# Kernel tuning notes

Measured on AMD Instinct MI355X. Metric: run time of the kernel, lower is better.

Reference implementation:

```python
import jax, jax.numpy as jnp
import numpy as np

N, E, DIN, H, EIN, EH, STEPS = 10000, 100000, 64, 64, 16, 128, 3


def setup_inputs() -> dict:
    key = jax.random.key(0)
    ks = jax.random.split(key, 8)
    n_feat = jax.random.normal(ks[0], (N, DIN), jnp.float32)
    e_feat = jax.random.normal(ks[1], (E, EIN), jnp.float32)
    src = jax.random.randint(ks[2], (E,), 0, N, jnp.int32)
    dst = jax.random.randint(ks[3], (E,), 0, N, jnp.int32)
    W0 = jax.random.normal(ks[4], (DIN, H), jnp.float32) / np.sqrt(DIN)
    b0 = jnp.zeros((H,), jnp.float32)
    We1 = jax.random.normal(ks[5], (EIN, EH), jnp.float32) / np.sqrt(EIN)
    be1 = jnp.zeros((EH,), jnp.float32)
    # small scale so per-edge HxH weight matrices keep activations stable
    We2 = jax.random.normal(ks[6], (EH, H * H), jnp.float32) * 0.02
    be2 = jnp.zeros((H * H,), jnp.float32)
    conv_bias = jnp.zeros((H,), jnp.float32)
    gamma = jnp.ones((H,), jnp.float32)
    beta = jnp.zeros((H,), jnp.float32)
    return {"n_feat": n_feat, "e_feat": e_feat, "src": src, "dst": dst,
            "W0": W0, "b0": b0, "We1": We1, "be1": be1, "We2": We2,
            "be2": be2, "conv_bias": conv_bias, "gamma": gamma, "beta": beta}


def reference(n_feat, e_feat, src, dst, W0, b0, We1, be1, We2, be2, conv_bias, gamma, beta):
    n = n_feat.shape[0]
    h = W0.shape[1]
    out = jax.nn.relu(n_feat @ W0 + b0)  # [N,H]
    # edge network (eval mode: dropout = identity); e_feat is fixed so the
    # per-edge weight matrices are identical each step -> compute once.
    w_edge = (jax.nn.relu(e_feat @ We1 + be1) @ We2 + be2).reshape(-1, h, h)  # [E,H,H]
    for _ in range(STEPS):
        msg = jnp.einsum('ei,eio->eo', out[src], w_edge)  # gather + per-edge matmul
        agg = jax.ops.segment_sum(msg, dst, num_segments=n)  # scatter-sum to dst
        out = jax.nn.relu(agg + conv_bias)
    # BatchNorm1d over nodes (training-mode batch statistics)
    mean = jnp.mean(out, axis=0)
    var = jnp.var(out, axis=0)
    return (out - mean) * jax.lax.rsqrt(var + 1e-5) * gamma + beta
```

## Files before the change

kernel.cpp:

```cpp
#include <hip/hip_runtime.h>
#include <stdint.h>

#define DIN   64
#define HDIM  64
#define EIN   16
#define EHID  128
#define HH    4096
#define TC    8256
#define STEPS 3

typedef short bf16x8 __attribute__((ext_vector_type(8)));
typedef float f32x4  __attribute__((ext_vector_type(4)));

__device__ __forceinline__ unsigned short f32_to_bf16(float f) {
    union { float f; uint32_t u; } v; v.f = f;
    uint32_t r = v.u + 0x7fffu + ((v.u >> 16) & 1u);
    return (unsigned short)(r >> 16);
}
__device__ __forceinline__ float bfu_to_f(unsigned short u) {
    union { uint32_t u; float f; } v; v.u = (uint32_t)u << 16; return v.f;
}

__global__ void k_node_mlp(const float* __restrict__ nf, const float* __restrict__ W0,
                           const float* __restrict__ b0, float* __restrict__ outb,
                           unsigned short* __restrict__ outbf, int n_nodes) {
    __shared__ float w0s[DIN * HDIM];
    int tid = threadIdx.x;
    for (int i = tid; i < DIN * HDIM; i += 256) w0s[i] = W0[i];
    __syncthreads();
    int node = blockIdx.x * 4 + (tid >> 6);
    int o = tid & 63;
    if (node >= n_nodes) return;
    float xr = nf[node * DIN + o];
    float acc = b0[o];
#pragma unroll 8
    for (int i = 0; i < DIN; ++i)
        acc += __shfl(xr, i, 64) * w0s[i * HDIM + o];
    float v = fmaxf(acc, 0.f);
    outb[node * HDIM + o] = v;
    outbf[node * HDIM + o] = f32_to_bf16(v);
}

__global__ void k_edge_mlp(const float* __restrict__ ef, const float* __restrict__ We1,
                           const float* __restrict__ be1, unsigned short* __restrict__ h, int n_edges) {
    __shared__ float w1s[EIN * EHID];
    __shared__ float xs[16 * EIN];
    int t = threadIdx.x;
    int e0 = blockIdx.x * 16;
#pragma unroll
    for (int i = t; i < EIN * EHID; i += 256) w1s[i] = We1[i];
    xs[t] = ef[(size_t)e0 * EIN + t];
    __syncthreads();
    int g = t >> 4, c0 = (t & 15) * 8;
    int edge = e0 + g;
    if (edge >= n_edges) return;
    float acc[8];
#pragma unroll
    for (int j = 0; j < 8; ++j) acc[j] = be1[c0 + j];
#pragma unroll
    for (int i = 0; i < EIN; ++i) {
        float xi = xs[g * EIN + i];
#pragma unroll
        for (int j = 0; j < 8; ++j) acc[j] += xi * w1s[i * EHID + c0 + j];
    }
    uint32_t p0 = f32_to_bf16(fmaxf(acc[0], 0.f)) | ((uint32_t)f32_to_bf16(fmaxf(acc[1], 0.f)) << 16);
    uint32_t p1 = f32_to_bf16(fmaxf(acc[2], 0.f)) | ((uint32_t)f32_to_bf16(fmaxf(acc[3], 0.f)) << 16);
    uint32_t p2 = f32_to_bf16(fmaxf(acc[4], 0.f)) | ((uint32_t)f32_to_bf16(fmaxf(acc[5], 0.f)) << 16);
    uint32_t p3 = f32_to_bf16(fmaxf(acc[6], 0.f)) | ((uint32_t)f32_to_bf16(fmaxf(acc[7], 0.f)) << 16);
    uint4 pk = {p0, p1, p2, p3};
    *(uint4*)(h + (size_t)edge * EHID + c0) = pk;
}

__global__ void k_bmat(const float* __restrict__ We2, const float* __restrict__ be2,
                       unsigned short* __restrict__ BmatT) {
    int t = blockIdx.x * 256 + threadIdx.x;
    if (t >= TC * 64) return;
    int c = t >> 6, i = t & 63;
    int g = c & 63;
    int m = (c & ~63) + 4 * (g & 15) + (g >> 4);
    float v;
    if (m < 8192) {
        int k = ((m >> 11) << 5) | (m & 31);
        int o = (m >> 5) & 63;
        v = We2[k * HH + i * 64 + o];
    } else {
        v = be2[i * 64 + (m - 8192)];
    }
    BmatT[t] = f32_to_bf16(v);
}

__global__ void k_T(const unsigned short* __restrict__ outbf, const unsigned short* __restrict__ BmatT,
                    unsigned short* __restrict__ T, int n0, int n1) {
    int wave = threadIdx.x >> 6, lane = threadIdx.x & 63;
    int r = lane & 15, q = lane >> 4;
    int eb = n0 + blockIdx.y * 64;
    int cb = blockIdx.x * 256 + wave * 64;
    f32x4 acc[4][4] = {};
#pragma unroll
    for (int s = 0; s < 2; ++s) {
        bf16x8 afr[4], bfr[4];
#pragma unroll
        for (int mt = 0; mt < 4; ++mt) {
            int e = eb + mt * 16 + r;
            if (e >= n1) e = n1 - 1;
            afr[mt] = *(const bf16x8*)(outbf + (size_t)e * 64 + s * 32 + q * 8);
        }
#pragma unroll
        for (int nt = 0; nt < 4; ++nt) {
            int c = cb + nt * 16 + r;
            if (c >= TC) c = 0;
            bfr[nt] = *(const bf16x8*)(BmatT + (size_t)c * 64 + s * 32 + q * 8);
        }
#pragma unroll
        for (int mt = 0; mt < 4; ++mt)
#pragma unroll
            for (int nt = 0; nt < 4; ++nt)
                acc[mt][nt] = __builtin_amdgcn_mfma_f32_16x16x32_bf16(afr[mt], bfr[nt], acc[mt][nt], 0, 0, 0);
    }
    if (cb >= TC) return;
#pragma unroll
    for (int mt = 0; mt < 4; ++mt)
#pragma unroll
        for (int rg = 0; rg < 4; ++rg) {
            int n = eb + mt * 16 + q * 4 + rg;
            if (n >= n1) continue;
            ushort4 pk;
            pk.x = f32_to_bf16(acc[mt][0][rg]);
            pk.y = f32_to_bf16(acc[mt][1][rg]);
            pk.z = f32_to_bf16(acc[mt][2][rg]);
            pk.w = f32_to_bf16(acc[mt][3][rg]);
            *(ushort4*)(T + (size_t)(n - n0) * TC + cb + 4 * r) = pk;
        }
}

__global__ void k_msg(const unsigned short* __restrict__ h, const unsigned short* __restrict__ T,
                      const int* __restrict__ offS, const int* __restrict__ permS,
                      float* __restrict__ msg, int n0, int n1) {
    int wave = threadIdx.x >> 6, lane = threadIdx.x & 63;
    int n = n0 + blockIdx.x * 4 + wave;
    if (n >= n1) return;
    int beg = offS[n], end = offS[n + 1];
    if (beg == end) return;
    int r = lane & 15, q = lane >> 4;
    const unsigned short* Tb = T + (size_t)(n - n0) * TC;
    float bias[4];
#pragma unroll
    for (int nt = 0; nt < 4; ++nt)
        bias[nt] = bfu_to_f(Tb[8192 + nt * 16 + r]);
    for (int j0 = beg; j0 < end; j0 += 16) {
        int jc = j0 + r; if (jc >= end) jc = end - 1;
        int e = permS[jc];
        const unsigned short* he = h + (size_t)e * EHID;
        f32x4 acc[4] = {};
#pragma unroll
        for (int s = 0; s < 4; ++s) {
            bf16x8 afr = *(const bf16x8*)(he + s * 32 + q * 8);
#pragma unroll
            for (int nt = 0; nt < 4; ++nt) {
                bf16x8 bfr = *(const bf16x8*)(Tb + s * 2048 + (nt * 16 + r) * 32 + q * 8);
                acc[nt] = __builtin_amdgcn_mfma_f32_16x16x32_bf16(afr, bfr, acc[nt], 0, 0, 0);
            }
        }
#pragma unroll
        for (int rg = 0; rg < 4; ++rg) {
            int jr = j0 + q * 4 + rg;
            if (jr >= end) continue;
            int er = permS[jr];
#pragma unroll
            for (int nt = 0; nt < 4; ++nt)
                msg[(size_t)er * 64 + nt * 16 + r] = acc[nt][rg] + bias[nt];
        }
    }
}

__global__ void k_hist(const int* __restrict__ src, const int* __restrict__ dst,
                       int* __restrict__ cntS, int* __restrict__ cntD, int n_edges) {
    int e = blockIdx.x * 256 + threadIdx.x;
    if (e >= n_edges) return;
    atomicAdd(&cntS[src[e]], 1);
    atomicAdd(&cntD[dst[e]], 1);
}

__global__ void k_scan(const int* __restrict__ cntS, const int* __restrict__ cntD,
                       int* __restrict__ offS, int* __restrict__ offD,
                       int* __restrict__ curS, int* __restrict__ curD, int n, int total) {
    const int* cnt = blockIdx.x ? cntD : cntS;
    int* off = blockIdx.x ? offD : offS;
    int* cur = blockIdx.x ? curD : curS;
    __shared__ int part[256];
    int tid = threadIdx.x;
    int chunk = (n + 255) / 256;
    int c0 = tid * chunk, c1 = c0 + chunk; if (c1 > n) c1 = n; if (c0 > n) c0 = n;
    int s = 0;
    for (int i = c0; i < c1; ++i) s += cnt[i];
    part[tid] = s;
    __syncthreads();
    for (int st = 1; st < 256; st <<= 1) {
        int v = (tid >= st) ? part[tid - st] : 0;
        __syncthreads();
        part[tid] += v;
        __syncthreads();
    }
    int run = tid ? part[tid - 1] : 0;
    for (int i = c0; i < c1; ++i) { off[i] = run; cur[i] = run; run += cnt[i]; }
    if (tid == 0) off[n] = total;
}

__global__ void k_perm(const int* __restrict__ src, const int* __restrict__ dst,
                       int* __restrict__ curS, int* __restrict__ curD,
                       int* __restrict__ permS, int* __restrict__ permD, int n_edges) {
    int e = blockIdx.x * 256 + threadIdx.x;
    if (e >= n_edges) return;
    permS[atomicAdd(&curS[src[e]], 1)] = e;
    permD[atomicAdd(&curD[dst[e]], 1)] = e;
}

__global__ void k_agg(const float* __restrict__ msg, const int* __restrict__ offD,
                      const int* __restrict__ permD, const float* __restrict__ cbias,
                      float* __restrict__ outb, unsigned short* __restrict__ outbf, int n_nodes) {
    int wave = threadIdx.x >> 6, lane = threadIdx.x & 63;
    int d = blockIdx.x * 4 + wave;
    if (d >= n_nodes) return;
    float acc = 0.f;
    int end = offD[d + 1];
    for (int j = offD[d]; j < end; ++j)
        acc += msg[(size_t)permD[j] * 64 + lane];
    float v = fmaxf(acc + cbias[lane], 0.f);
    outb[(size_t)d * 64 + lane] = v;
    outbf[(size_t)d * 64 + lane] = f32_to_bf16(v);
}

__global__ void k_bn_stats(const float* __restrict__ out, float* __restrict__ stat, int n_nodes) {
    __shared__ float s1[256], s2[256];
    int tid = threadIdx.x;
    int f = tid & 63, g = tid >> 6;
    float sum = 0.f, ss = 0.f;
    for (int r = blockIdx.x * 4 + g; r < n_nodes; r += 256) {
        float v = out[r * HDIM + f];
        sum += v; ss += v * v;
    }
    s1[tid] = sum; s2[tid] = ss;
    __syncthreads();
    if (tid < 64) {
        float A = s1[tid] + s1[64 + tid] + s1[128 + tid] + s1[192 + tid];
        float B = s2[tid] + s2[64 + tid] + s2[128 + tid] + s2[192 + tid];
        atomicAdd(&stat[tid], A);
        atomicAdd(&stat[64 + tid], B);
    }
}

__global__ void k_bn_final(const float* __restrict__ stat, const float* __restrict__ gamma,
                           const float* __restrict__ beta, float* __restrict__ sc, int n_nodes) {
    int f = threadIdx.x;
    if (f >= 64) return;
    float mean = stat[f] / n_nodes;
    float var  = stat[64 + f] / n_nodes - mean * mean;
    float inv  = rsqrtf(var + 1e-5f);
    float scale = gamma[f] * inv;
    sc[f] = scale;
    sc[64 + f] = beta[f] - mean * scale;
}

__global__ void k_bn_apply(const float* __restrict__ out, const float* __restrict__ sc,
                           float* __restrict__ y, int n) {
    int t = blockIdx.x * 256 + threadIdx.x;
    if (t >= n) return;
    int f = t & 63;
    y[t] = out[t] * sc[f] + sc[64 + f];
}

extern "C" void kernel_launch(void* const* d_in, const int* in_sizes, int n_in,
                              void* d_out, int out_size, void* d_ws, size_t ws_size,
                              hipStream_t stream) {
    const float* nf    = (const float*)d_in[0];
    const float* ef    = (const float*)d_in[1];
    const int*   src   = (const int*)d_in[2];
    const int*   dst   = (const int*)d_in[3];
    const float* W0    = (const float*)d_in[4];
    const float* b0    = (const float*)d_in[5];
    const float* We1   = (const float*)d_in[6];
    const float* be1   = (const float*)d_in[7];
    const float* We2   = (const float*)d_in[8];
    const float* be2   = (const float*)d_in[9];
    const float* cbias = (const float*)d_in[10];
    const float* gamma = (const float*)d_in[11];
    const float* beta  = (const float*)d_in[12];
    (void)n_in; (void)out_size;

    int n_nodes = in_sizes[0] / DIN;
    int n_edges = in_sizes[2];

    char* ws = (char*)d_ws;
    size_t off = 0;
    auto carve = [&](size_t bytes) -> void* {
        void* p = ws + off;
        off = (off + bytes + 255) & ~(size_t)255;
        return p;
    };
    unsigned short* h     = (unsigned short*)carve((size_t)n_edges * EHID * 2);
    float*          msg   = (float*)carve((size_t)n_edges * 64 * 4);
    float*          outb  = (float*)carve((size_t)n_nodes * HDIM * 4);
    unsigned short* outbf = (unsigned short*)carve((size_t)n_nodes * HDIM * 2);
    unsigned short* BmatT = (unsigned short*)carve((size_t)TC * 64 * 2);
    int*            offS  = (int*)carve((size_t)(n_nodes + 1) * 4);
    int*            offD  = (int*)carve((size_t)(n_nodes + 1) * 4);
    int*            curS  = (int*)carve((size_t)n_nodes * 4);
    int*            curD  = (int*)carve((size_t)n_nodes * 4);
    int*            permS = (int*)carve((size_t)n_edges * 4);
    int*            permD = (int*)carve((size_t)n_edges * 4);
    float*          stat  = (float*)carve(128 * 4 + (size_t)2 * n_nodes * 4);
    int*            cntS  = (int*)(stat + 128);
    int*            cntD  = cntS + n_nodes;
    float*          sc    = (float*)carve(128 * 4);
    unsigned short* T     = (unsigned short*)(ws + off);
    size_t avail = ws_size > off ? ws_size - off : 0;
    long tcap = (long)(avail / ((size_t)TC * 2));
    if (tcap > n_nodes) tcap = n_nodes;
    if (tcap < 64) tcap = 64;
    long half = (((long)n_nodes + 1) / 2 + 63) & ~63L;
    long tchunk = tcap < half ? tcap : half;

    hipMemsetAsync(stat, 0, 128 * 4 + (size_t)2 * n_nodes * 4, stream);

    k_node_mlp<<<dim3((n_nodes + 3) / 4), 256, 0, stream>>>(nf, W0, b0, outb, outbf, n_nodes);
    k_edge_mlp<<<dim3((n_edges + 15) / 16), 256, 0, stream>>>(ef, We1, be1, h, n_edges);
    k_bmat<<<dim3((TC * 64 + 255) / 256), 256, 0, stream>>>(We2, be2, BmatT);
    k_hist<<<dim3((n_edges + 255) / 256), 256, 0, stream>>>(src, dst, cntS, cntD, n_edges);
    k_scan<<<dim3(2), 256, 0, stream>>>(cntS, cntD, offS, offD, curS, curD, n_nodes, n_edges);
    k_perm<<<dim3((n_edges + 255) / 256), 256, 0, stream>>>(src, dst, curS, curD, permS, permD, n_edges);

    for (int step = 0; step < STEPS; ++step) {
        for (long n0 = 0; n0 < n_nodes; n0 += tchunk) {
            long n1 = n0 + tchunk; if (n1 > n_nodes) n1 = n_nodes;
            long cnt = n1 - n0;
            k_T<<<dim3((TC + 255) / 256, (cnt + 63) / 64), 256, 0, stream>>>(
                outbf, BmatT, T, (int)n0, (int)n1);
            k_msg<<<dim3((cnt + 3) / 4), 256, 0, stream>>>(
                h, T, offS, permS, msg, (int)n0, (int)n1);
        }
        k_agg<<<dim3((n_nodes + 3) / 4), 256, 0, stream>>>(msg, offD, permD, cbias, outb, outbf, n_nodes);
    }

    k_bn_stats<<<dim3(64), 256, 0, stream>>>(outb, stat, n_nodes);
    k_bn_final<<<dim3(1), 64, 0, stream>>>(stat, gamma, beta, sc, n_nodes);
    k_bn_apply<<<dim3((n_nodes * HDIM + 255) / 256), 256, 0, stream>>>(
        outb, sc, (float*)d_out, n_nodes * HDIM);
}
```

Before: 512.4 us.

## Merge prologue kernels, fold BN finalize into apply, retile k_T

Folds the node MLP, edge MLP, weight-matrix repack and degree histogram into one launch that dispatches on block index, and folds the BatchNorm finalize kernel into the apply kernel. Together these drop four launches. k_T now keeps the B fragments in registers and loops over 128 rows per block (8 M-tiles) instead of 64. This halves the grid in y and reuses B loads across more rows, but the bigger blocks may leave some compute units idle.

```diff
diff --git a/kernel.cpp b/kernel.cpp
--- a/kernel.cpp
+++ b/kernel.cpp
@@ -21,116 +21,122 @@
     union { uint32_t u; float f; } v; v.u = (uint32_t)u << 16; return v.f;
 }
 
-__global__ void k_node_mlp(const float* __restrict__ nf, const float* __restrict__ W0,
-                           const float* __restrict__ b0, float* __restrict__ outb,
-                           unsigned short* __restrict__ outbf, int n_nodes) {
-    __shared__ float w0s[DIN * HDIM];
-    int tid = threadIdx.x;
-    for (int i = tid; i < DIN * HDIM; i += 256) w0s[i] = W0[i];
-    __syncthreads();
-    int node = blockIdx.x * 4 + (tid >> 6);
-    int o = tid & 63;
-    if (node >= n_nodes) return;
-    float xr = nf[node * DIN + o];
-    float acc = b0[o];
+__global__ void k_pro(const float* __restrict__ nf, const float* __restrict__ W0,
+                      const float* __restrict__ b0, float* __restrict__ outb,
+                      unsigned short* __restrict__ outbf,
+                      const float* __restrict__ ef, const float* __restrict__ We1,
+                      const float* __restrict__ be1, unsigned short* __restrict__ h,
+                      const float* __restrict__ We2, const float* __restrict__ be2,
+                      unsigned short* __restrict__ BmatT,
+                      const int* __restrict__ src, const int* __restrict__ dst,
+                      int* __restrict__ cntS, int* __restrict__ cntD,
+                      int n_nodes, int n_edges, int nbN, int nbE, int nbB) {
+    __shared__ float smem[DIN * HDIM];
+    int b = blockIdx.x, tid = threadIdx.x;
+    if (b < nbN) {
+        for (int i = tid; i < DIN * HDIM; i += 256) smem[i] = W0[i];
+        __syncthreads();
+        int node = b * 4 + (tid >> 6);
+        int o = tid & 63;
+        if (node >= n_nodes) return;
+        float xr = nf[node * DIN + o];
+        float acc = b0[o];
 #pragma unroll 8
-    for (int i = 0; i < DIN; ++i)
-        acc += __shfl(xr, i, 64) * w0s[i * HDIM + o];
-    float v = fmaxf(acc, 0.f);
-    outb[node * HDIM + o] = v;
-    outbf[node * HDIM + o] = f32_to_bf16(v);
-}
-
-__global__ void k_edge_mlp(const float* __restrict__ ef, const float* __restrict__ We1,
-                           const float* __restrict__ be1, unsigned short* __restrict__ h, int n_edges) {
-    __shared__ float w1s[EIN * EHID];
-    __shared__ float xs[16 * EIN];
-    int t = threadIdx.x;
-    int e0 = blockIdx.x * 16;
-#pragma unroll
-    for (int i = t; i < EIN * EHID; i += 256) w1s[i] = We1[i];
-    xs[t] = ef[(size_t)e0 * EIN + t];
-    __syncthreads();
-    int g = t >> 4, c0 = (t & 15) * 8;
-    int edge = e0 + g;
-    if (edge >= n_edges) return;
-    float acc[8];
-#pragma unroll
-    for (int j = 0; j < 8; ++j) acc[j] = be1[c0 + j];
-#pragma unroll
-    for (int i = 0; i < EIN; ++i) {
-        float xi = xs[g * EIN + i];
-#pragma unroll
-        for (int j = 0; j < 8; ++j) acc[j] += xi * w1s[i * EHID + c0 + j];
-    }
-    uint32_t p0 = f32_to_bf16(fmaxf(acc[0], 0.f)) | ((uint32_t)f32_to_bf16(fmaxf(acc[1], 0.f)) << 16);
-    uint32_t p1 = f32_to_bf16(fmaxf(acc[2], 0.f)) | ((uint32_t)f32_to_bf16(fmaxf(acc[3], 0.f)) << 16);
-    uint32_t p2 = f32_to_bf16(fmaxf(acc[4], 0.f)) | ((uint32_t)f32_to_bf16(fmaxf(acc[5], 0.f)) << 16);
-    uint32_t p3 = f32_to_bf16(fmaxf(acc[6], 0.f)) | ((uint32_t)f32_to_bf16(fmaxf(acc[7], 0.f)) << 16);
-    uint4 pk = {p0, p1, p2, p3};
-    *(uint4*)(h + (size_t)edge * EHID + c0) = pk;
-}
-
-__global__ void k_bmat(const float* __restrict__ We2, const float* __restrict__ be2,
-                       unsigned short* __restrict__ BmatT) {
-    int t = blockIdx.x * 256 + threadIdx.x;
-    if (t >= TC * 64) return;
-    int c = t >> 6, i = t & 63;
-    int g = c & 63;
-    int m = (c & ~63) + 4 * (g & 15) + (g >> 4);
-    float v;
-    if (m < 8192) {
-        int k = ((m >> 11) << 5) | (m & 31);
-        int o = (m >> 5) & 63;
-        v = We2[k * HH + i * 64 + o];
+        for (int i = 0; i < DIN; ++i)
+            acc += __shfl(xr, i, 64) * smem[i * HDIM + o];
+        float v = fmaxf(acc, 0.f);
+        outb[node * HDIM + o] = v;
+        outbf[node * HDIM + o] = f32_to_bf16(v);
+    } else if (b < nbN + nbE) {
+        float* w1s = smem;
+        float* xs  = smem + EIN * EHID;
+        int e0 = (b - nbN) * 16;
+#pragma unroll
+        for (int i = tid; i < EIN * EHID; i += 256) w1s[i] = We1[i];
+        xs[tid] = ef[(size_t)e0 * EIN + tid];
+        __syncthreads();
+        int g = tid >> 4, c0 = (tid & 15) * 8;
+        int edge = e0 + g;
+        if (edge >= n_edges) return;
+        float acc[8];
+#pragma unroll
+        for (int j = 0; j < 8; ++j) acc[j] = be1[c0 + j];
+#pragma unroll
+        for (int i = 0; i < EIN; ++i) {
+            float xi = xs[g * EIN + i];
+#pragma unroll
+            for (int j = 0; j < 8; ++j) acc[j] += xi * w1s[i * EHID + c0 + j];
+        }
+        uint32_t p0 = f32_to_bf16(fmaxf(acc[0], 0.f)) | ((uint32_t)f32_to_bf16(fmaxf(acc[1], 0.f)) << 16);
+        uint32_t p1 = f32_to_bf16(fmaxf(acc[2], 0.f)) | ((uint32_t)f32_to_bf16(fmaxf(acc[3], 0.f)) << 16);
+        uint32_t p2 = f32_to_bf16(fmaxf(acc[4], 0.f)) | ((uint32_t)f32_to_bf16(fmaxf(acc[5], 0.f)) << 16);
+        uint32_t p3 = f32_to_bf16(fmaxf(acc[6], 0.f)) | ((uint32_t)f32_to_bf16(fmaxf(acc[7], 0.f)) << 16);
+        uint4 pk = {p0, p1, p2, p3};
+        *(uint4*)(h + (size_t)edge * EHID + c0) = pk;
+    } else if (b < nbN + nbE + nbB) {
+        int t = (b - nbN - nbE) * 256 + tid;
+        if (t >= TC * 64) return;
+        int c = t >> 6, i = t & 63;
+        int g = c & 63;
+        int m = (c & ~63) + 4 * (g & 15) + (g >> 4);
+        float v;
+        if (m < 8192) {
+            int k = ((m >> 11) << 5) | (m & 31);
+            int o = (m >> 5) & 63;
+            v = We2[k * HH + i * 64 + o];
+        } else {
+            v = be2[i * 64 + (m - 8192)];
+        }
+        BmatT[t] = f32_to_bf16(v);
     } else {
-        v = be2[i * 64 + (m - 8192)];
-    }
-    BmatT[t] = f32_to_bf16(v);
+        int e = (b - nbN - nbE - nbB) * 256 + tid;
+        if (e >= n_edges) return;
+        atomicAdd(&cntS[src[e]], 1);
+        atomicAdd(&cntD[dst[e]], 1);
+    }
 }
 
 __global__ void k_T(const unsigned short* __restrict__ outbf, const unsigned short* __restrict__ BmatT,
                     unsigned short* __restrict__ T, int n0, int n1) {
     int wave = threadIdx.x >> 6, lane = threadIdx.x & 63;
     int r = lane & 15, q = lane >> 4;
-    int eb = n0 + blockIdx.y * 64;
+    int eb = n0 + blockIdx.y * 128;
     int cb = blockIdx.x * 256 + wave * 64;
-    f32x4 acc[4][4] = {};
-#pragma unroll
-    for (int s = 0; s < 2; ++s) {
-        bf16x8 afr[4], bfr[4];
-#pragma unroll
-        for (int mt = 0; mt < 4; ++mt) {
-            int e = eb + mt * 16 + r;
-            if (e >= n1) e = n1 - 1;
-            afr[mt] = *(const bf16x8*)(outbf + (size_t)e * 64 + s * 32 + q * 8);
-        }
+    bf16x8 bfr[4][2];
+#pragma unroll
+    for (int nt = 0; nt < 4; ++nt) {
+        int c = cb + nt * 16 + r;
+        if (c >= TC) c = 0;
+        size_t cofs = (size_t)c * 64;
+        bfr[nt][0] = *(const bf16x8*)(BmatT + cofs + q * 8);
+        bfr[nt][1] = *(const bf16x8*)(BmatT + cofs + 32 + q * 8);
+    }
+    bool cok = (cb < TC);
+#pragma unroll
+    for (int mt = 0; mt < 8; ++mt) {
+        int e = eb + mt * 16 + r;
+        if (e >= n1) e = n1 - 1;
+        bf16x8 afr0 = *(const bf16x8*)(outbf + (size_t)e * 64 + q * 8);
+        bf16x8 afr1 = *(const bf16x8*)(outbf + (size_t)e * 64 + 32 + q * 8);
+        f32x4 acc[4] = {};
 #pragma unroll
         for (int nt = 0; nt < 4; ++nt) {
-            int c = cb + nt * 16 + r;
-            if (c >= TC) c = 0;
-            bfr[nt] = *(const bf16x8*)(BmatT + (size_t)c * 64 + s * 32 + q * 8);
-        }
-#pragma unroll
-        for (int mt = 0; mt < 4; ++mt)
-#pragma unroll
-            for (int nt = 0; nt < 4; ++nt)
-                acc[mt][nt] = __builtin_amdgcn_mfma_f32_16x16x32_bf16(afr[mt], bfr[nt], acc[mt][nt], 0, 0, 0);
-    }
-    if (cb >= TC) return;
-#pragma unroll
-    for (int mt = 0; mt < 4; ++mt)
+            acc[nt] = __builtin_amdgcn_mfma_f32_16x16x32_bf16(afr0, bfr[nt][0], acc[nt], 0, 0, 0);
+            acc[nt] = __builtin_amdgcn_mfma_f32_16x16x32_bf16(afr1, bfr[nt][1], acc[nt], 0, 0, 0);
+        }
+        if (!cok) continue;
 #pragma unroll
         for (int rg = 0; rg < 4; ++rg) {
             int n = eb + mt * 16 + q * 4 + rg;
             if (n >= n1) continue;
             ushort4 pk;
-            pk.x = f32_to_bf16(acc[mt][0][rg]);
-            pk.y = f32_to_bf16(acc[mt][1][rg]);
-            pk.z = f32_to_bf16(acc[mt][2][rg]);
-            pk.w = f32_to_bf16(acc[mt][3][rg]);
+            pk.x = f32_to_bf16(acc[0][rg]);
+            pk.y = f32_to_bf16(acc[1][rg]);
+            pk.z = f32_to_bf16(acc[2][rg]);
+            pk.w = f32_to_bf16(acc[3][rg]);
             *(ushort4*)(T + (size_t)(n - n0) * TC + cb + 4 * r) = pk;
         }
+    }
 }
 
 __global__ void k_msg(const unsigned short* __restrict__ h, const unsigned short* __restrict__ T,
@@ -171,14 +177,6 @@
                 msg[(size_t)er * 64 + nt * 16 + r] = acc[nt][rg] + bias[nt];
         }
     }
-}
-
-__global__ void k_hist(const int* __restrict__ src, const int* __restrict__ dst,
-                       int* __restrict__ cntS, int* __restrict__ cntD, int n_edges) {
-    int e = blockIdx.x * 256 + threadIdx.x;
-    if (e >= n_edges) return;
-    atomicAdd(&cntS[src[e]], 1);
-    atomicAdd(&cntD[dst[e]], 1);
 }
 
 __global__ void k_scan(const int* __restrict__ cntS, const int* __restrict__ cntD,
@@ -249,24 +247,18 @@
     }
 }
 
-__global__ void k_bn_final(const float* __restrict__ stat, const float* __restrict__ gamma,
-                           const float* __restrict__ beta, float* __restrict__ sc, int n_nodes) {
-    int f = threadIdx.x;
-    if (f >= 64) return;
+__global__ void k_bn_apply(const float* __restrict__ out, const float* __restrict__ stat,
+                           const float* __restrict__ gamma, const float* __restrict__ beta,
+                           float* __restrict__ y, int n, int n_nodes) {
+    int t = blockIdx.x * 256 + threadIdx.x;
+    if (t >= n) return;
+    int f = t & 63;
     float mean = stat[f] / n_nodes;
     float var  = stat[64 + f] / n_nodes - mean * mean;
     float inv  = rsqrtf(var + 1e-5f);
     float scale = gamma[f] * inv;
-    sc[f] = scale;
-    sc[64 + f] = beta[f] - mean * scale;
-}
-
-__global__ void k_bn_apply(const float* __restrict__ out, const float* __restrict__ sc,
-                           float* __restrict__ y, int n) {
-    int t = blockIdx.x * 256 + threadIdx.x;
-    if (t >= n) return;
-    int f = t & 63;
-    y[t] = out[t] * sc[f] + sc[64 + f];
+    float shift = beta[f] - mean * scale;
+    y[t] = out[t] * scale + shift;
 }
 
 extern "C" void kernel_launch(void* const* d_in, const int* in_sizes, int n_in,
@@ -311,7 +303,6 @@
     float*          stat  = (float*)carve(128 * 4 + (size_t)2 * n_nodes * 4);
     int*            cntS  = (int*)(stat + 128);
     int*            cntD  = cntS + n_nodes;
-    float*          sc    = (float*)carve(128 * 4);
     unsigned short* T     = (unsigned short*)(ws + off);
     size_t avail = ws_size > off ? ws_size - off : 0;
     long tcap = (long)(avail / ((size_t)TC * 2));
@@ -322,10 +313,13 @@
 
     hipMemsetAsync(stat, 0, 128 * 4 + (size_t)2 * n_nodes * 4, stream);
 
-    k_node_mlp<<<dim3((n_nodes + 3) / 4), 256, 0, stream>>>(nf, W0, b0, outb, outbf, n_nodes);
-    k_edge_mlp<<<dim3((n_edges + 15) / 16), 256, 0, stream>>>(ef, We1, be1, h, n_edges);
-    k_bmat<<<dim3((TC * 64 + 255) / 256), 256, 0, stream>>>(We2, be2, BmatT);
-    k_hist<<<dim3((n_edges + 255) / 256), 256, 0, stream>>>(src, dst, cntS, cntD, n_edges);
+    int nbN = (n_nodes + 3) / 4;
+    int nbE = (n_edges + 15) / 16;
+    int nbB = (TC * 64 + 255) / 256;
+    int nbH = (n_edges + 255) / 256;
+    k_pro<<<dim3(nbN + nbE + nbB + nbH), 256, 0, stream>>>(
+        nf, W0, b0, outb, outbf, ef, We1, be1, h, We2, be2, BmatT,
+        src, dst, cntS, cntD, n_nodes, n_edges, nbN, nbE, nbB);
     k_scan<<<dim3(2), 256, 0, stream>>>(cntS, cntD, offS, offD, curS, curD, n_nodes, n_edges);
     k_perm<<<dim3((n_edges + 255) / 256), 256, 0, stream>>>(src, dst, curS, curD, permS, permD, n_edges);
 
@@ -333,7 +327,7 @@
         for (long n0 = 0; n0 < n_nodes; n0 += tchunk) {
             long n1 = n0 + tchunk; if (n1 > n_nodes) n1 = n_nodes;
             long cnt = n1 - n0;
-            k_T<<<dim3((TC + 255) / 256, (cnt + 63) / 64), 256, 0, stream>>>(
+            k_T<<<dim3((TC + 255) / 256, (cnt + 127) / 128), 256, 0, stream>>>(
                 outbf, BmatT, T, (int)n0, (int)n1);
             k_msg<<<dim3((cnt + 3) / 4), 256, 0, stream>>>(
                 h, T, offS, permS, msg, (int)n0, (int)n1);
@@ -342,7 +336,6 @@
     }
 
     k_bn_stats<<<dim3(64), 256, 0, stream>>>(outb, stat, n_nodes);
-    k_bn_final<<<dim3(1), 64, 0, stream>>>(stat, gamma, beta, sc, n_nodes);
     k_bn_apply<<<dim3((n_nodes * HDIM + 255) / 256), 256, 0, stream>>>(
-        outb, sc, (float*)d_out, n_nodes * HDIM);
-}
+        outb, stat, gamma, beta, (float*)d_out, n_nodes * HDIM, n_nodes);
+}
```

After: 481.3 us. 6.1% less time.
